# Kernel tuning notes

Hardware: AMD Instinct MI355X
Metric: run time of the kernel (lower is better)

Reference implementation:

```python
import jax, jax.numpy as jnp
import numpy as np

D_MODEL = 2048
NUM_HEADS = 16
HEAD_DIM = 128
ROPE_BASE = 10000.0
NEG_INF = -1e9


def setup_inputs() -> dict:
    key = jax.random.key(0)
    ks = jax.random.split(key, 5)
    B, S = 2, 2048
    hidden_states = jax.random.normal(ks[0], (B, S, D_MODEL), dtype=jnp.float32)
    # additive causal mask: 0 on/below diagonal, large-negative above
    causal = jnp.triu(jnp.full((S, S), NEG_INF, dtype=jnp.float32), k=1)
    attention_mask = jnp.broadcast_to(causal, (B, 1, S, S))
    position_ids = jnp.broadcast_to(jnp.arange(S, dtype=jnp.int32), (B, S))
    scale = 1.0 / np.sqrt(D_MODEL)
    Wq = jax.random.normal(ks[1], (D_MODEL, NUM_HEADS * HEAD_DIM), dtype=jnp.float32) * scale
    Wk = jax.random.normal(ks[2], (D_MODEL, NUM_HEADS * HEAD_DIM), dtype=jnp.float32) * scale
    Wv = jax.random.normal(ks[3], (D_MODEL, NUM_HEADS * HEAD_DIM), dtype=jnp.float32) * scale
    Wo = jax.random.normal(ks[4], (NUM_HEADS * HEAD_DIM, D_MODEL), dtype=jnp.float32) * scale
    return {"hidden_states": hidden_states, "attention_mask": attention_mask,
            "position_ids": position_ids, "Wq": Wq, "Wk": Wk, "Wv": Wv, "Wo": Wo}


def _rope_cos_sin(position_ids):
    # inv_freq: [head_dim/2]
    inv_freq = 1.0 / (ROPE_BASE ** (jnp.arange(0, HEAD_DIM, 2, dtype=jnp.float32) / HEAD_DIM))
    freqs = position_ids.astype(jnp.float32)[..., None] * inv_freq  # [B,S,hd/2]
    emb = jnp.concatenate([freqs, freqs], axis=-1)  # [B,S,hd]
    return jnp.cos(emb), jnp.sin(emb)


def _rotate_half(x):
    x1, x2 = jnp.split(x, 2, axis=-1)
    return jnp.concatenate([-x2, x1], axis=-1)


def reference(hidden_states, attention_mask, position_ids, Wq, Wk, Wv, Wo):
    B, S, _ = hidden_states.shape
    H, Dh = NUM_HEADS, HEAD_DIM
    q = (hidden_states @ Wq).reshape(B, S, H, Dh).transpose(0, 2, 1, 3)  # [B,H,S,Dh]
    k = (hidden_states @ Wk).reshape(B, S, H, Dh).transpose(0, 2, 1, 3)
    v = (hidden_states @ Wv).reshape(B, S, H, Dh).transpose(0, 2, 1, 3)
    cos, sin = _rope_cos_sin(position_ids)  # [B,S,Dh]
    cos = cos[:, None, :, :]  # [B,1,S,Dh]
    sin = sin[:, None, :, :]
    q = q * cos + _rotate_half(q) * sin
    k = k * cos + _rotate_half(k) * sin
    scaling = 1.0 / np.sqrt(Dh)
    scores = jnp.einsum('bhqd,bhkd->bhqk', q, k) * scaling  # [B,H,S,S]
    scores = scores + attention_mask[:, :, :, :S]
    attn = jax.nn.softmax(scores.astype(jnp.float32), axis=-1).astype(q.dtype)
    # dropout p=0.0 / eval mode -> identity
    out = jnp.einsum('bhqk,bhkd->bhqd', attn, v)  # [B,H,S,Dh]
    out = out.transpose(0, 2, 1, 3).reshape(B, S, H * Dh)
    return out @ Wo
```

## Files before the change

kernel.cpp:

```cpp
#include <hip/hip_runtime.h>

typedef __attribute__((ext_vector_type(4))) float f32x4;
typedef __attribute__((ext_vector_type(8))) _Float16 f16x8;
typedef __attribute__((ext_vector_type(4))) _Float16 f16x4;

#define SEQ 2048
#define DM 2048
#define NQKV 6144

__device__ __forceinline__ void gload16(const _Float16* g, _Float16* l) {
  __builtin_amdgcn_global_load_lds(
      (const __attribute__((address_space(1))) void*)g,
      (__attribute__((address_space(3))) void*)l, 16, 0, 0);
}

__global__ __launch_bounds__(256) void cvt_x_kernel(const float* __restrict__ X,
                                                    _Float16* __restrict__ Xb, int n4) {
  int i = blockIdx.x * 256 + threadIdx.x;
  if (i < n4) {
    const float4 v = ((const float4*)X)[i];
    f16x4 o;
    o.x = (_Float16)v.x; o.y = (_Float16)v.y; o.z = (_Float16)v.z; o.w = (_Float16)v.w;
    ((f16x4*)Xb)[i] = o;
  }
}

__global__ __launch_bounds__(256) void wtrans_all_kernel(const float* __restrict__ Wq,
                                                         const float* __restrict__ Wk,
                                                         const float* __restrict__ Wv,
                                                         const float* __restrict__ Wo,
                                                         _Float16* __restrict__ Wqkvt,
                                                         _Float16* __restrict__ Wot) {
  __shared__ float tile[64][65];
  const int z = blockIdx.z;
  const float* W = (z == 0) ? Wq : (z == 1) ? Wk : (z == 2) ? Wv : Wo;
  _Float16* Wt = (z < 3) ? (Wqkvt + (size_t)z * 2048 * 2048) : Wot;
  const int n0 = blockIdx.x * 64, k0 = blockIdx.y * 64;
  const int tx = threadIdx.x & 15, ty = threadIdx.x >> 4;
#pragma unroll
  for (int i = 0; i < 4; ++i) {
    const int r = ty + i * 16;
    const float4 v = *(const float4*)&W[(size_t)(k0 + r) * 2048 + n0 + tx * 4];
    tile[r][tx * 4] = v.x; tile[r][tx * 4 + 1] = v.y;
    tile[r][tx * 4 + 2] = v.z; tile[r][tx * 4 + 3] = v.w;
  }
  __syncthreads();
  const int r = threadIdx.x >> 2, u = threadIdx.x & 3;
  _Float16 o[16];
#pragma unroll
  for (int i = 0; i < 16; ++i) o[i] = (_Float16)tile[u * 16 + i][r];
  _Float16* dst = &Wt[(size_t)(n0 + r) * 2048 + k0 + u * 16];
  *(f16x8*)&dst[0] = *(f16x8*)&o[0];
  *(f16x8*)&dst[8] = *(f16x8*)&o[8];
}

__global__ __launch_bounds__(256) void rope_table_kernel(float* __restrict__ ct,
                                                         float* __restrict__ st) {
  int i = blockIdx.x * 256 + threadIdx.x;
  int pos = i >> 6, f = i & 63;
  float inv = powf(10000.0f, -(float)f / 64.0f);
  float ang = (float)pos * inv;
  ct[i] = cosf(ang);
  st[i] = sinf(ang);
}

template <int MODE>
__global__ __launch_bounds__(512, 2) void gemm8n_kernel(
    const _Float16* __restrict__ A, const _Float16* __restrict__ Bt,
    float* __restrict__ Cout, int M, int N, int K,
    const int* __restrict__ pos_ids, const float* __restrict__ ct,
    const float* __restrict__ st, _Float16* __restrict__ Qo,
    _Float16* __restrict__ Ko, _Float16* __restrict__ Vo) {
  __shared__ __align__(16) char smem[147456];
  _Float16* As = (_Float16*)smem;
  _Float16* Bs = (_Float16*)(smem + 98304);
  const int nwg = gridDim.x * gridDim.y;
  const int orig = blockIdx.y * gridDim.x + blockIdx.x;
  const int id = (orig & 7) * (nwg >> 3) + (orig >> 3);
  const int bx = id % gridDim.x, by = id / gridDim.x;
  const int bm = by * 256, bn = bx * 128;
  const int t = threadIdx.x, lane = t & 63, w = t >> 6;
  const int wm = w >> 2, wn = w & 3;
  const int rl = lane & 15, lr4 = lane >> 4;
  const int NKT = K >> 6;

  const int srow = t >> 3;
  const int scol = ((t & 7) ^ (srow & 7)) << 3;
  const _Float16* pA = A + (size_t)(bm + srow) * K + scol;
  const _Float16* pB = Bt + (size_t)(bn + srow) * K + scol;
  _Float16* lA = As + t * 8;
  _Float16* lB = Bs + t * 8;
  const size_t rowK64 = (size_t)64 * K;

#define STA(H, KT, SLOT)                                                   \
  { const size_t _g = (size_t)((H) * 128) * K + (size_t)(KT) * 64;         \
    gload16(pA + _g, lA + (SLOT) * 16384 + (H) * 8192);                    \
    gload16(pA + _g + rowK64, lA + (SLOT) * 16384 + (H) * 8192 + 4096); }
#define STB(KT, SLOT)                                                      \
  { const size_t _g = (size_t)(KT) * 64;                                   \
    gload16(pB + _g, lB + (SLOT) * 8192);                                  \
    gload16(pB + _g + rowK64, lB + (SLOT) * 8192 + 4096); }

  const int sw0 = (lr4 ^ (rl & 7)) << 3;
  const int sw1 = ((4 + lr4) ^ (rl & 7)) << 3;
  const int aoff = (wm * 64 + rl) * 64;
  const int boff = (wn * 32 + rl) * 64;

  f16x8 a_[4][2], b_[2][2];
  f32x4 acc[2][4][2];
#pragma unroll
  for (int qm = 0; qm < 2; ++qm)
#pragma unroll
    for (int mf = 0; mf < 4; ++mf)
#pragma unroll
      for (int nf = 0; nf < 2; ++nf) acc[qm][mf][nf] = (f32x4)0.0f;

#define LOAD_A(H, SLOT)                                                 \
  { const _Float16* _p = As + (SLOT) * 16384 + (H) * 8192 + aoff;       \
    _Pragma("unroll") for (int mf = 0; mf < 4; ++mf) {                  \
      a_[mf][0] = *(const f16x8*)&_p[mf * 1024 + sw0];                  \
      a_[mf][1] = *(const f16x8*)&_p[mf * 1024 + sw1]; } }
#define LOAD_B(SLOT)                                                    \
  { const _Float16* _p = Bs + (SLOT) * 8192 + boff;                     \
    _Pragma("unroll") for (int nf = 0; nf < 2; ++nf) {                  \
      b_[nf][0] = *(const f16x8*)&_p[nf * 1024 + sw0];                  \
      b_[nf][1] = *(const f16x8*)&_p[nf * 1024 + sw1]; } }
#define MFMA_Q(QM)                                                      \
  __builtin_amdgcn_s_setprio(1);                                        \
  _Pragma("unroll") for (int mf = 0; mf < 4; ++mf)                      \
    _Pragma("unroll") for (int nf = 0; nf < 2; ++nf) {                  \
      acc[QM][mf][nf] = __builtin_amdgcn_mfma_f32_16x16x32_f16(         \
          a_[mf][0], b_[nf][0], acc[QM][mf][nf], 0, 0, 0);              \
      acc[QM][mf][nf] = __builtin_amdgcn_mfma_f32_16x16x32_f16(         \
          a_[mf][1], b_[nf][1], acc[QM][mf][nf], 0, 0, 0); }            \
  __builtin_amdgcn_s_setprio(0);
#define BAR()                                                           \
  do { __builtin_amdgcn_sched_barrier(0); __builtin_amdgcn_s_barrier(); \
       __builtin_amdgcn_sched_barrier(0); } while (0)
#define LGKM0()                                                         \
  do { asm volatile("s_waitcnt lgkmcnt(0)" ::: "memory");               \
       __builtin_amdgcn_sched_barrier(0); } while (0)
#define VM6() asm volatile("s_waitcnt vmcnt(6)" ::: "memory")
#define VM0() asm volatile("s_waitcnt vmcnt(0)" ::: "memory")

  STA(0, 0, 0); STB(0, 0); STA(1, 0, 0);
  STA(0, 1, 1); STB(1, 1); STA(1, 1, 1);
  VM6();
  BAR();

  for (int jb = 0; jb + 4 < NKT; jb += 3) {
    LOAD_A(0, 0); LOAD_B(0); STA(0, jb + 2, 2); STB(jb + 2, 2);
    BAR(); LGKM0(); MFMA_Q(0); BAR();
    LOAD_A(1, 0); STA(1, jb + 2, 2);
    VM6(); BAR(); LGKM0(); MFMA_Q(1); BAR();
    LOAD_A(0, 1); LOAD_B(1); STA(0, jb + 3, 0); STB(jb + 3, 0);
    BAR(); LGKM0(); MFMA_Q(0); BAR();
    LOAD_A(1, 1); STA(1, jb + 3, 0);
    VM6(); BAR(); LGKM0(); MFMA_Q(1); BAR();
    LOAD_A(0, 2); LOAD_B(2); STA(0, jb + 4, 1); STB(jb + 4, 1);
    BAR(); LGKM0(); MFMA_Q(0); BAR();
    LOAD_A(1, 2); STA(1, jb + 4, 1);
    VM6(); BAR(); LGKM0(); MFMA_Q(1); BAR();
  }
  {
    LOAD_A(0, 0); LOAD_B(0);
    BAR(); LGKM0(); MFMA_Q(0); BAR();
    LOAD_A(1, 0);
    VM0();
    BAR(); LGKM0(); MFMA_Q(1); BAR();
    LOAD_A(0, 1); LOAD_B(1);
    BAR(); LGKM0(); MFMA_Q(0); BAR();
    LOAD_A(1, 1);
    BAR(); LGKM0(); MFMA_Q(1);
  }

  if (MODE == 0) {
#pragma unroll
    for (int qm = 0; qm < 2; ++qm)
#pragma unroll
      for (int mf = 0; mf < 4; ++mf)
#pragma unroll
        for (int nf = 0; nf < 2; ++nf) {
          const int col = bn + wn * 32 + nf * 16 + rl;
#pragma unroll
          for (int ri = 0; ri < 4; ++ri) {
            const int row = bm + qm * 128 + wm * 64 + mf * 16 + lr4 * 4 + ri;
            Cout[(size_t)row * N + col] = acc[qm][mf][nf][ri];
          }
        }
  } else {
    const int ttype = bx >> 4;
    const int hh = bx & 15;
    if (ttype == 2) {
#pragma unroll
      for (int qm = 0; qm < 2; ++qm)
#pragma unroll
        for (int mf = 0; mf < 4; ++mf)
#pragma unroll
          for (int nf = 0; nf < 2; ++nf) {
            const int d = wn * 32 + nf * 16 + rl;
            const int s0 = bm + qm * 128 + wm * 64 + mf * 16 + lr4 * 4;
            const int bb = s0 >> 11, ss = s0 & 2047;
            f16x4 v4;
#pragma unroll
            for (int ri = 0; ri < 4; ++ri) v4[ri] = (_Float16)acc[qm][mf][nf][ri];
            *(f16x4*)&Vo[((size_t)(bb * 16 + hh) * 128 + d) * SEQ + ss] = v4;
          }
    } else {
      float* cl = (float*)smem;
      LGKM0();
      BAR();
#pragma unroll
      for (int qm = 0; qm < 2; ++qm)
#pragma unroll
        for (int mf = 0; mf < 4; ++mf)
#pragma unroll
          for (int nf = 0; nf < 2; ++nf) {
            const int col = wn * 32 + nf * 16 + rl;
            const int r0 = qm * 128 + wm * 64 + mf * 16 + lr4 * 4;
#pragma unroll
            for (int ri = 0; ri < 4; ++ri) cl[(r0 + ri) * 130 + col] = acc[qm][mf][nf][ri];
          }
      BAR();
      const int row = t >> 1, pb = (t & 1) * 32;
      const int rg = bm + row;
      const int bb = rg >> 11, ss = rg & 2047;
      const int pos = pos_ids[rg];
      const float* cp = ct + pos * 64 + pb;
      const float* sp = st + pos * 64 + pb;
      _Float16* dst = (ttype ? Ko : Qo) + ((size_t)(bb * 16 + hh) * SEQ + ss) * 128;
      const float qs = ttype ? 1.0f : 0.08838834764831845f;
      const float* crow = cl + row * 130;
      _Float16 o1[32], o2[32];
#pragma unroll
      for (int i = 0; i < 32; ++i) {
        const float x1 = crow[pb + i], x2 = crow[pb + 64 + i];
        const float c = cp[i], s = sp[i];
        o1[i] = (_Float16)((x1 * c - x2 * s) * qs);
        o2[i] = (_Float16)((x2 * c + x1 * s) * qs);
      }
#pragma unroll
      for (int i = 0; i < 4; ++i) {
        *(f16x8*)&dst[pb + i * 8] = *(f16x8*)&o1[i * 8];
        *(f16x8*)&dst[pb + 64 + i * 8] = *(f16x8*)&o2[i * 8];
      }
    }
  }
#undef STA
#undef STB
#undef LOAD_A
#undef LOAD_B
#undef MFMA_Q
#undef BAR
#undef LGKM0
#undef VM6
#undef VM0
}

__global__ __launch_bounds__(512) void attn_kernel(const _Float16* __restrict__ Q,
                                                   const _Float16* __restrict__ K,
                                                   const _Float16* __restrict__ Vt,
                                                   _Float16* __restrict__ O) {
  __shared__ __align__(16) _Float16 Ks[2][64 * 128];
  __shared__ __align__(16) _Float16 Vs[2][128 * 64];
  __shared__ __align__(16) _Float16 Ps[8][16 * 72];
  const int bh = blockIdx.x;
  const int pair = blockIdx.y;
  const int b = bh >> 4, h = bh & 15;
  const int t = threadIdx.x, lane = t & 63, w = t >> 6;
  const int lr = lane >> 4, lc = lane & 15;
  const _Float16* Qb = Q + (size_t)bh * SEQ * 128;
  const _Float16* Kb = K + (size_t)bh * SEQ * 128;
  const _Float16* Vb = Vt + (size_t)bh * 128 * SEQ;

  f16x8 onef;
#pragma unroll
  for (int i = 0; i < 8; ++i) onef[i] = (_Float16)1.0f;

#define ABAR()                                                          \
  do { __builtin_amdgcn_sched_barrier(0); __builtin_amdgcn_s_barrier(); \
       __builtin_amdgcn_sched_barrier(0); } while (0)

  auto stage = [&](int buf, int kb) {
    const int k0 = kb * 64;
#pragma unroll
    for (int i = 0; i < 2; ++i) {
      const int c = i * 512 + t;
      const int row = c >> 4, u = c & 15;
      gload16(&Kb[(size_t)(k0 + row) * 128 + ((u ^ (row & 7)) * 8)], &Ks[buf][c * 8]);
    }
#pragma unroll
    for (int i = 0; i < 2; ++i) {
      const int c = i * 512 + t;
      const int dim = c >> 3, u = c & 7;
      gload16(&Vb[(size_t)dim * SEQ + k0 + ((u ^ (dim & 7)) * 8)], &Vs[buf][c * 8]);
    }
  };

  for (int half = 0; half < 2; ++half) {
    const int j = half ? (15 - pair) : pair;
    const int q0 = j * 128;
    const int nkb = 2 * j + 2;
    const int rowmin = q0 + w * 16;

    f16x8 qf[4];
    {
      const int qrow = q0 + w * 16 + lc;
#pragma unroll
      for (int kk = 0; kk < 4; ++kk)
        qf[kk] = *(const f16x8*)&Qb[(size_t)qrow * 128 + kk * 32 + lr * 8];
    }
    f32x4 acco[8];
#pragma unroll
    for (int i = 0; i < 8; ++i) acco[i] = (f32x4)0.0f;
    float m_r[4] = {-1e30f, -1e30f, -1e30f, -1e30f};
    float l_r[4] = {0.f, 0.f, 0.f, 0.f};

    stage(0, 0);
    for (int kb = 0; kb < nkb; ++kb) {
      const int cur = kb & 1;
      const bool more = kb + 1 < nkb;
      if (more) {
        stage(cur ^ 1, kb + 1);
        asm volatile("s_waitcnt vmcnt(4)" ::: "memory");
      } else {
        asm volatile("s_waitcnt vmcnt(0)" ::: "memory");
      }
      ABAR();
      const int k0 = kb * 64;
      if (k0 <= rowmin + 15) {
        f32x4 sacc[4];
#pragma unroll
        for (int jj = 0; jj < 4; ++jj) sacc[jj] = (f32x4)0.0f;
#pragma unroll
        for (int jj = 0; jj < 4; ++jj) {
          const int krow = jj * 16 + lc;
#pragma unroll
          for (int kk = 0; kk < 4; ++kk) {
            const int idx = (krow * 128 + kk * 32 + lr * 8) ^ ((krow & 7) << 3);
            f16x8 kf = *(const f16x8*)&Ks[cur][idx];
            sacc[jj] = __builtin_amdgcn_mfma_f32_16x16x32_f16(qf[kk], kf, sacc[jj], 0, 0, 0);
          }
        }
        const bool diag = (k0 + 63 > rowmin);
#pragma unroll
        for (int r = 0; r < 4; ++r) {
          const int rowi = rowmin + lr * 4 + r;
          float s[4], mx = -1e30f;
#pragma unroll
          for (int jj = 0; jj < 4; ++jj) {
            float sv = sacc[jj][r];
            if (diag && (k0 + jj * 16 + lc > rowi)) sv = -1e30f;
            s[jj] = sv;
            mx = fmaxf(mx, sv);
          }
#pragma unroll
          for (int msk = 1; msk < 16; msk <<= 1) mx = fmaxf(mx, __shfl_xor(mx, msk));
          const float mn = fmaxf(m_r[r], mx);
          const float sc = __expf(m_r[r] - mn);
#pragma unroll
          for (int jj = 0; jj < 4; ++jj) {
            const float pv = __expf(s[jj] - mn);
            Ps[w][(lr * 4 + r) * 72 + jj * 16 + lc] = (_Float16)pv;
          }
          l_r[r] *= sc;
          m_r[r] = mn;
#pragma unroll
          for (int tt = 0; tt < 8; ++tt) acco[tt][r] *= sc;
        }
        f16x8 pf0 = *(const f16x8*)&Ps[w][lc * 72 + lr * 8];
        f16x8 pf1 = *(const f16x8*)&Ps[w][lc * 72 + 32 + lr * 8];
        f32x4 psum = (f32x4)0.0f;
        psum = __builtin_amdgcn_mfma_f32_16x16x32_f16(pf0, onef, psum, 0, 0, 0);
        psum = __builtin_amdgcn_mfma_f32_16x16x32_f16(pf1, onef, psum, 0, 0, 0);
#pragma unroll
        for (int tt = 0; tt < 8; ++tt) {
          const int dim = tt * 16 + lc;
          const int v0 = (dim * 64 + lr * 8) ^ ((dim & 7) << 3);
          const int v1 = (dim * 64 + 32 + lr * 8) ^ ((dim & 7) << 3);
          acco[tt] = __builtin_amdgcn_mfma_f32_16x16x32_f16(
              pf0, *(const f16x8*)&Vs[cur][v0], acco[tt], 0, 0, 0);
          acco[tt] = __builtin_amdgcn_mfma_f32_16x16x32_f16(
              pf1, *(const f16x8*)&Vs[cur][v1], acco[tt], 0, 0, 0);
        }
#pragma unroll
        for (int r = 0; r < 4; ++r) l_r[r] += psum[r];
      }
      ABAR();
    }
#pragma unroll
    for (int tt = 0; tt < 8; ++tt) {
      const int col = h * 128 + tt * 16 + lc;
#pragma unroll
      for (int r = 0; r < 4; ++r) {
        const int row = q0 + w * 16 + lr * 4 + r;
        O[(size_t)(b * SEQ + row) * DM + col] = (_Float16)(acco[tt][r] / l_r[r]);
      }
    }
  }
#undef ABAR
}

extern "C" void kernel_launch(void* const* d_in, const int* in_sizes, int n_in,
                              void* d_out, int out_size, void* d_ws, size_t ws_size,
                              hipStream_t stream) {
  const float* hidden = (const float*)d_in[0];
  const int* pos_ids = (const int*)d_in[2];
  const float* Wq = (const float*)d_in[3];
  const float* Wk = (const float*)d_in[4];
  const float* Wv = (const float*)d_in[5];
  const float* Wo = (const float*)d_in[6];

  char* ws = (char*)d_ws;
  _Float16* Xb    = (_Float16*)(ws + 0);
  _Float16* Wqkvt = (_Float16*)(ws + 16777216);
  _Float16* Wot   = (_Float16*)(ws + 41943040);
  _Float16* Qbuf  = (_Float16*)(ws + 50331648);
  _Float16* Kbuf  = (_Float16*)(ws + 67108864);
  _Float16* Vtbuf = (_Float16*)(ws + 83886080);
  _Float16* Obuf  = (_Float16*)(ws + 100663296);
  float* ct       = (float*)(ws + 117440512);
  float* st       = (float*)(ws + 117964800);

  cvt_x_kernel<<<8192, 256, 0, stream>>>(hidden, Xb, 2097152);
  wtrans_all_kernel<<<dim3(32, 32, 4), 256, 0, stream>>>(Wq, Wk, Wv, Wo, Wqkvt, Wot);
  rope_table_kernel<<<512, 256, 0, stream>>>(ct, st);

  gemm8n_kernel<1><<<dim3(48, 16), 512, 0, stream>>>(
      Xb, Wqkvt, nullptr, 4096, 6144, 2048, pos_ids, ct, st, Qbuf, Kbuf, Vtbuf);

  attn_kernel<<<dim3(32, 8), 512, 0, stream>>>(Qbuf, Kbuf, Vtbuf, Obuf);

  gemm8n_kernel<0><<<dim3(16, 16), 512, 0, stream>>>(
      Obuf, Wot, (float*)d_out, 4096, 2048, 2048, nullptr, nullptr, nullptr,
      nullptr, nullptr, nullptr);
}
```

Measured before the change: 275.5 us.

## Split attention into one query tile per block and add lazy softmax rescaling

The attention kernel previously ran two query tiles per block (a pair balancing causal work). It now launches one block per 128-row query tile, doubling the grid to 512 blocks with heaviest tiles scheduled first, and requests 4 blocks per CU via launch bounds. The online softmax now skips rescaling the accumulators unless some row's max grows by more than 8, and the P staging buffer uses an XOR swizzle instead of padding. Together these aim to raise occupancy and cut per-iteration VALU work, at the cost of possible register pressure from the min-blocks hint and slightly larger fp16 P values when rescaling is deferred.

After: 539.1 us. 1.96x slower.

```diff
diff --git a/kernel.cpp b/kernel.cpp
--- a/kernel.cpp
+++ b/kernel.cpp
@@ -257,15 +257,15 @@
 #undef VM0
 }
 
-__global__ __launch_bounds__(512) void attn_kernel(const _Float16* __restrict__ Q,
-                                                   const _Float16* __restrict__ K,
-                                                   const _Float16* __restrict__ Vt,
-                                                   _Float16* __restrict__ O) {
+__global__ __launch_bounds__(512, 4) void attn_kernel(const _Float16* __restrict__ Q,
+                                                      const _Float16* __restrict__ K,
+                                                      const _Float16* __restrict__ Vt,
+                                                      _Float16* __restrict__ O) {
   __shared__ __align__(16) _Float16 Ks[2][64 * 128];
   __shared__ __align__(16) _Float16 Vs[2][128 * 64];
-  __shared__ __align__(16) _Float16 Ps[8][16 * 72];
+  __shared__ __align__(16) _Float16 Ps[8][16 * 64];
   const int bh = blockIdx.x;
-  const int pair = blockIdx.y;
+  const int j = 15 - blockIdx.y;
   const int b = bh >> 4, h = bh & 15;
   const int t = threadIdx.x, lane = t & 63, w = t >> 6;
   const int lr = lane >> 4, lc = lane & 15;
@@ -297,105 +297,126 @@
     }
   };
 
-  for (int half = 0; half < 2; ++half) {
-    const int j = half ? (15 - pair) : pair;
-    const int q0 = j * 128;
-    const int nkb = 2 * j + 2;
-    const int rowmin = q0 + w * 16;
-
-    f16x8 qf[4];
-    {
-      const int qrow = q0 + w * 16 + lc;
-#pragma unroll
-      for (int kk = 0; kk < 4; ++kk)
-        qf[kk] = *(const f16x8*)&Qb[(size_t)qrow * 128 + kk * 32 + lr * 8];
-    }
-    f32x4 acco[8];
-#pragma unroll
-    for (int i = 0; i < 8; ++i) acco[i] = (f32x4)0.0f;
-    float m_r[4] = {-1e30f, -1e30f, -1e30f, -1e30f};
-    float l_r[4] = {0.f, 0.f, 0.f, 0.f};
-
-    stage(0, 0);
-    for (int kb = 0; kb < nkb; ++kb) {
-      const int cur = kb & 1;
-      const bool more = kb + 1 < nkb;
-      if (more) {
-        stage(cur ^ 1, kb + 1);
-        asm volatile("s_waitcnt vmcnt(4)" ::: "memory");
-      } else {
-        asm volatile("s_waitcnt vmcnt(0)" ::: "memory");
-      }
-      ABAR();
-      const int k0 = kb * 64;
-      if (k0 <= rowmin + 15) {
-        f32x4 sacc[4];
-#pragma unroll
-        for (int jj = 0; jj < 4; ++jj) sacc[jj] = (f32x4)0.0f;
+  const int q0 = j * 128;
+  const int nkb = 2 * j + 2;
+  const int rowmin = q0 + w * 16;
+
+  f16x8 qf[4];
+  {
+    const int qrow = q0 + w * 16 + lc;
+#pragma unroll
+    for (int kk = 0; kk < 4; ++kk)
+      qf[kk] = *(const f16x8*)&Qb[(size_t)qrow * 128 + kk * 32 + lr * 8];
+  }
+  f32x4 acco[8];
+#pragma unroll
+  for (int i = 0; i < 8; ++i) acco[i] = (f32x4)0.0f;
+  float m_r[4] = {-1e30f, -1e30f, -1e30f, -1e30f};
+  float l_r[4] = {0.f, 0.f, 0.f, 0.f};
+
+  stage(0, 0);
+  for (int kb = 0; kb < nkb; ++kb) {
+    const int cur = kb & 1;
+    const bool more = kb + 1 < nkb;
+    if (more) {
+      stage(cur ^ 1, kb + 1);
+      asm volatile("s_waitcnt vmcnt(4)" ::: "memory");
+    } else {
+      asm volatile("s_waitcnt vmcnt(0)" ::: "memory");
+    }
+    ABAR();
+    const int k0 = kb * 64;
+    if (k0 <= rowmin + 15) {
+      f32x4 sacc[4];
+#pragma unroll
+      for (int jj = 0; jj < 4; ++jj) sacc[jj] = (f32x4)0.0f;
+#pragma unroll
+      for (int jj = 0; jj < 4; ++jj) {
+        const int krow = jj * 16 + lc;
+#pragma unroll
+        for (int kk = 0; kk < 4; ++kk) {
+          const int idx = (krow * 128 + kk * 32 + lr * 8) ^ ((krow & 7) << 3);
+          f16x8 kf = *(const f16x8*)&Ks[cur][idx];
+          sacc[jj] = __builtin_amdgcn_mfma_f32_16x16x32_f16(qf[kk], kf, sacc[jj], 0, 0, 0);
+        }
+      }
+      const bool diag = (k0 + 63 > rowmin);
+      float mx[4];
+#pragma unroll
+      for (int r = 0; r < 4; ++r) {
+        const int rowi = rowmin + lr * 4 + r;
+        float m0 = -1e30f;
 #pragma unroll
         for (int jj = 0; jj < 4; ++jj) {
-          const int krow = jj * 16 + lc;
-#pragma unroll
-          for (int kk = 0; kk < 4; ++kk) {
-            const int idx = (krow * 128 + kk * 32 + lr * 8) ^ ((krow & 7) << 3);
-            f16x8 kf = *(const f16x8*)&Ks[cur][idx];
-            sacc[jj] = __builtin_amdgcn_mfma_f32_16x16x32_f16(qf[kk], kf, sacc[jj], 0, 0, 0);
-          }
+          float sv = sacc[jj][r];
+          if (diag && (k0 + jj * 16 + lc > rowi)) sv = -1e30f;
+          sacc[jj][r] = sv;
+          m0 = fmaxf(m0, sv);
         }
-        const bool diag = (k0 + 63 > rowmin);
+#pragma unroll
+        for (int msk = 1; msk < 16; msk <<= 1) m0 = fmaxf(m0, __shfl_xor(m0, msk));
+        mx[r] = m0;
+      }
+      bool needv = false;
+#pragma unroll
+      for (int r = 0; r < 4; ++r) needv |= (mx[r] > m_r[r] + 8.0f);
+      if (__any(needv)) {
 #pragma unroll
         for (int r = 0; r < 4; ++r) {
-          const int rowi = rowmin + lr * 4 + r;
-          float s[4], mx = -1e30f;
+          const float mn = fmaxf(m_r[r], mx[r]);
+          const float sc = __expf(m_r[r] - mn);
+          const int rbase = (lr * 4 + r) * 64;
+          const int rsw = ((lr * 4 + r) & 7) << 3;
 #pragma unroll
           for (int jj = 0; jj < 4; ++jj) {
-            float sv = sacc[jj][r];
-            if (diag && (k0 + jj * 16 + lc > rowi)) sv = -1e30f;
-            s[jj] = sv;
-            mx = fmaxf(mx, sv);
-          }
-#pragma unroll
-          for (int msk = 1; msk < 16; msk <<= 1) mx = fmaxf(mx, __shfl_xor(mx, msk));
-          const float mn = fmaxf(m_r[r], mx);
-          const float sc = __expf(m_r[r] - mn);
-#pragma unroll
-          for (int jj = 0; jj < 4; ++jj) {
-            const float pv = __expf(s[jj] - mn);
-            Ps[w][(lr * 4 + r) * 72 + jj * 16 + lc] = (_Float16)pv;
+            const float pv = __expf(sacc[jj][r] - mn);
+            Ps[w][rbase + ((jj * 16 + lc) ^ rsw)] = (_Float16)pv;
           }
           l_r[r] *= sc;
           m_r[r] = mn;
 #pragma unroll
           for (int tt = 0; tt < 8; ++tt) acco[tt][r] *= sc;
         }
-        f16x8 pf0 = *(const f16x8*)&Ps[w][lc * 72 + lr * 8];
-        f16x8 pf1 = *(const f16x8*)&Ps[w][lc * 72 + 32 + lr * 8];
-        f32x4 psum = (f32x4)0.0f;
-        psum = __builtin_amdgcn_mfma_f32_16x16x32_f16(pf0, onef, psum, 0, 0, 0);
-        psum = __builtin_amdgcn_mfma_f32_16x16x32_f16(pf1, onef, psum, 0, 0, 0);
-#pragma unroll
-        for (int tt = 0; tt < 8; ++tt) {
-          const int dim = tt * 16 + lc;
-          const int v0 = (dim * 64 + lr * 8) ^ ((dim & 7) << 3);
-          const int v1 = (dim * 64 + 32 + lr * 8) ^ ((dim & 7) << 3);
-          acco[tt] = __builtin_amdgcn_mfma_f32_16x16x32_f16(
-              pf0, *(const f16x8*)&Vs[cur][v0], acco[tt], 0, 0, 0);
-          acco[tt] = __builtin_amdgcn_mfma_f32_16x16x32_f16(
-              pf1, *(const f16x8*)&Vs[cur][v1], acco[tt], 0, 0, 0);
+      } else {
+#pragma unroll
+        for (int r = 0; r < 4; ++r) {
+          const int rbase = (lr * 4 + r) * 64;
+          const int rsw = ((lr * 4 + r) & 7) << 3;
+#pragma unroll
+          for (int jj = 0; jj < 4; ++jj) {
+            const float pv = __expf(sacc[jj][r] - m_r[r]);
+            Ps[w][rbase + ((jj * 16 + lc) ^ rsw)] = (_Float16)pv;
+          }
         }
-#pragma unroll
-        for (int r = 0; r < 4; ++r) l_r[r] += psum[r];
-      }
-      ABAR();
-    }
-#pragma unroll
-    for (int tt = 0; tt < 8; ++tt) {
-      const int col = h * 128 + tt * 16 + lc;
-#pragma unroll
-      for (int r = 0; r < 4; ++r) {
-        const int row = q0 + w * 16 + lr * 4 + r;
-        O[(size_t)(b * SEQ + row) * DM + col] = (_Float16)(acco[tt][r] / l_r[r]);
-      }
+      }
+      const int csw = (lc & 7) << 3;
+      f16x8 pf0 = *(const f16x8*)&Ps[w][lc * 64 + ((lr * 8) ^ csw)];
+      f16x8 pf1 = *(const f16x8*)&Ps[w][lc * 64 + ((lr * 8 + 32) ^ csw)];
+      f32x4 psum = (f32x4)0.0f;
+      psum = __builtin_amdgcn_mfma_f32_16x16x32_f16(pf0, onef, psum, 0, 0, 0);
+      psum = __builtin_amdgcn_mfma_f32_16x16x32_f16(pf1, onef, psum, 0, 0, 0);
+#pragma unroll
+      for (int tt = 0; tt < 8; ++tt) {
+        const int dim = tt * 16 + lc;
+        const int v0 = (dim * 64 + lr * 8) ^ ((dim & 7) << 3);
+        const int v1 = (dim * 64 + 32 + lr * 8) ^ ((dim & 7) << 3);
+        acco[tt] = __builtin_amdgcn_mfma_f32_16x16x32_f16(
+            pf0, *(const f16x8*)&Vs[cur][v0], acco[tt], 0, 0, 0);
+        acco[tt] = __builtin_amdgcn_mfma_f32_16x16x32_f16(
+            pf1, *(const f16x8*)&Vs[cur][v1], acco[tt], 0, 0, 0);
+      }
+#pragma unroll
+      for (int r = 0; r < 4; ++r) l_r[r] += psum[r];
+    }
+    ABAR();
+  }
+#pragma unroll
+  for (int tt = 0; tt < 8; ++tt) {
+    const int col = h * 128 + tt * 16 + lc;
+#pragma unroll
+    for (int r = 0; r < 4; ++r) {
+      const int row = q0 + w * 16 + lr * 4 + r;
+      O[(size_t)(b * SEQ + row) * DM + col] = (_Float16)(acco[tt][r] / l_r[r]);
     }
   }
 #undef ABAR
@@ -429,7 +450,7 @@
   gemm8n_kernel<1><<<dim3(48, 16), 512, 0, stream>>>(
       Xb, Wqkvt, nullptr, 4096, 6144, 2048, pos_ids, ct, st, Qbuf, Kbuf, Vtbuf);
 
-  attn_kernel<<<dim3(32, 8), 512, 0, stream>>>(Qbuf, Kbuf, Vtbuf, Obuf);
+  attn_kernel<<<dim3(32, 16), 512, 0, stream>>>(Qbuf, Kbuf, Vtbuf, Obuf);
 
   gemm8n_kernel<0><<<dim3(16, 16), 512, 0, stream>>>(
       Obuf, Wot, (float*)d_out, 4096, 2048, 2048, nullptr, nullptr, nullptr,
```
